# Performance work log

Hardware: AMD Instinct MI355X
Metric: run time of the kernel (lower is better)

## Reference

```python
import jax, jax.numpy as jnp
import numpy as np

N = 50000   # nodes
E = 800000  # edges
G = 64      # graphs in the batch
DIN = 128
DOUT = 256


def _lin(key, fan_in, fan_out):
    s = 1.0 / np.sqrt(fan_in)
    kw, kb = jax.random.split(key)
    W = jax.random.uniform(kw, (fan_in, fan_out), jnp.float32, -s, s)
    b = jax.random.uniform(kb, (fan_out,), jnp.float32, -s, s)
    return W, b


def setup_inputs() -> dict:
    key = jax.random.key(0)
    ks = jax.random.split(key, 12)
    x = jax.random.normal(ks[0], (N, DIN), jnp.float32)
    edge_index = jax.random.randint(ks[1], (2, E), 0, N, dtype=jnp.int64)
    batch = jnp.sort(jax.random.randint(ks[2], (N,), 0, G, dtype=jnp.int64))
    W1, b1 = _lin(ks[3], DIN, 128)
    W2, b2 = _lin(ks[4], 128, 128)
    W3, b3 = _lin(ks[5], 128, 128)
    A1, ba1 = _lin(ks[6], DIN, 64)
    A2, ba2 = _lin(ks[7], 64, 32)
    A3, ba3 = _lin(ks[8], 32, 1)
    M1, bm1 = _lin(ks[9], 128, 128)
    M2, bm2 = _lin(ks[10], 128, DOUT)
    return dict(x=x, edge_index=edge_index, batch=batch,
                W1=W1, b1=b1, W2=W2, b2=b2, W3=W3, b3=b3,
                A1=A1, ba1=ba1, A2=A2, ba2=ba2, A3=A3, ba3=ba3,
                M1=M1, bm1=bm1, M2=M2, bm2=bm2)


def _gcn_norm(edge_index, n, dtype):
    # GCNConv default: add self-loops, symmetric normalization D^-1/2 (A+I) D^-1/2
    loop = jnp.arange(n, dtype=edge_index.dtype)
    src = jnp.concatenate([edge_index[0], loop])
    dst = jnp.concatenate([edge_index[1], loop])
    deg = jax.ops.segment_sum(jnp.ones_like(dst, dtype), dst, num_segments=n)
    dinv = jnp.where(deg > 0, jax.lax.rsqrt(deg), 0.0)
    return src, dst, dinv[src] * dinv[dst]


def _gcn(h, W, b, src, dst, norm, n):
    h = h @ W                                   # [N, F_out]
    msg = h[src] * norm[:, None]                # gather + scale (memory bound)
    return jax.ops.segment_sum(msg, dst, num_segments=n) + b


def _segment_softmax(w, batch, g):
    # per-graph softmax (PyG softmax): stabilize with segment max
    m = jax.ops.segment_max(w, batch, num_segments=g)
    e = jnp.exp(w - m[batch])
    s = jax.ops.segment_sum(e, batch, num_segments=g)
    return e / (s[batch] + 1e-16)


def reference(x, edge_index, batch,
              W1, b1, W2, b2, W3, b3,
              A1, ba1, A2, ba2, A3, ba3,
              M1, bm1, M2, bm2):
    n = x.shape[0]
    src, dst, norm = _gcn_norm(edge_index, n, x.dtype)
    relu = jax.nn.relu
    # feature branch
    f = relu(_gcn(x, W1, b1, src, dst, norm, n))
    f = relu(_gcn(f, W2, b2, src, dst, norm, n))
    f = relu(_gcn(f, W3, b3, src, dst, norm, n))
    # attention branch
    w = relu(_gcn(x, A1, ba1, src, dst, norm, n))
    w = relu(_gcn(w, A2, ba2, src, dst, norm, n))
    w = relu(_gcn(w, A3, ba3, src, dst, norm, n))   # [N, 1]
    w = _segment_softmax(w, batch, G)
    # attention-weighted sum pooling per graph
    pooled = jax.ops.segment_sum(f * w, batch, num_segments=G)  # [G, 128]
    # MLP([128,128,256], batch_norm=False): Linear+ReLU, plain last Linear
    out = relu(pooled @ M1 + bm1) @ M2 + bm2
    return out
```

## Files before the change

kernel.cpp:

```cpp
#include <hip/hip_runtime.h>
#include <hip/hip_fp16.h>
#include <math.h>


#define DIN 128
#define FH  128
#define DOUT 256
#define NBUK 128
#define SUBN 512
#define IMGCAP 16384
#define ECAP 16384

typedef float f4 __attribute__((ext_vector_type(4)));
typedef float f32x4 __attribute__((ext_vector_type(4)));
typedef _Float16 h8v __attribute__((ext_vector_type(8)));
typedef _Float16 h4v __attribute__((ext_vector_type(4)));


__global__ __launch_bounds__(256) void scan1_kernel(const int* __restrict__ cnt,
        int* __restrict__ bsum, float* __restrict__ dinv, int n) {
    __shared__ int sm[256];
    int tid = threadIdx.x;
    int base = blockIdx.x * 512;
    int a = (base + tid < n) ? cnt[base + tid] : 0;
    int b = (base + 256 + tid < n) ? cnt[base + 256 + tid] : 0;
    if (base + tid < n)       dinv[base + tid]       = rsqrtf((float)(a + 1));
    if (base + 256 + tid < n) dinv[base + 256 + tid] = rsqrtf((float)(b + 1));
    sm[tid] = a + b;
    __syncthreads();
    for (int off = 128; off > 0; off >>= 1) {
        if (tid < off) sm[tid] += sm[tid + off];
        __syncthreads();
    }
    if (tid == 0) bsum[blockIdx.x] = sm[0];
}

__global__ void scan2_kernel(const int* __restrict__ bsum, int* __restrict__ boff,
                             int* __restrict__ rpN, int nb) {
    if (threadIdx.x == 0) {
        int run = 0;
        for (int i = 0; i < nb; ++i) { boff[i] = run; run += bsum[i]; }
        *rpN = run;
    }
}

__global__ __launch_bounds__(256) void scan3_kernel(const int* __restrict__ cnt,
        const int* __restrict__ boff, int* __restrict__ rp, int n) {
    __shared__ int sm[256];
    int tid = threadIdx.x;
    int base = blockIdx.x * 512;
    int i0 = base + 2 * tid;
    int c0 = (i0 < n) ? cnt[i0] : 0;
    int c1 = (i0 + 1 < n) ? cnt[i0 + 1] : 0;
    int ps = c0 + c1;
    sm[tid] = ps;
    __syncthreads();
    for (int off = 1; off < 256; off <<= 1) {
        int v = (tid >= off) ? sm[tid - off] : 0;
        __syncthreads();
        sm[tid] += v;
        __syncthreads();
    }
    int excl = sm[tid] - ps + boff[blockIdx.x];
    if (i0 < n) rp[i0] = excl;
    if (i0 + 1 < n) rp[i0 + 1] = excl + c0;
}

__global__ __launch_bounds__(256) void ebucket_kernel(const int* __restrict__ src,
        const int* __restrict__ dst, int* __restrict__ bcur,
        unsigned long long* __restrict__ entries, int E, int shift) {
    __shared__ int lcnt[NBUK], lscan[NBUK], lbase[NBUK], lcur[NBUK];
    __shared__ unsigned long long stage[2048];
    const int tid = threadIdx.x;
    const int e0 = blockIdx.x * 2048;
    if (tid < NBUK) { lcnt[tid] = 0; lcur[tid] = 0; }
    __syncthreads();
    int s_[8], d_[8];
    #pragma unroll
    for (int k = 0; k < 8; ++k) {
        int e = e0 + k * 256 + tid;
        if (e < E) {
            s_[k] = src[e];
            d_[k] = dst[e];
            atomicAdd(&lcnt[d_[k] >> shift], 1);
        } else {
            d_[k] = -1;
        }
    }
    __syncthreads();
    if (tid < NBUK) lscan[tid] = lcnt[tid];
    __syncthreads();
    for (int off = 1; off < NBUK; off <<= 1) {
        int v = 0;
        if (tid < NBUK && tid >= off) v = lscan[tid - off];
        __syncthreads();
        if (tid < NBUK) lscan[tid] += v;
        __syncthreads();
    }
    if (tid < NBUK) {
        lscan[tid] -= lcnt[tid];
        lbase[tid] = lcnt[tid] ? atomicAdd(&bcur[tid], lcnt[tid]) : 0;
    }
    __syncthreads();
    #pragma unroll
    for (int k = 0; k < 8; ++k) {
        if (d_[k] >= 0) {
            int b = d_[k] >> shift;
            int pos = lscan[b] + atomicAdd(&lcur[b], 1);
            stage[pos] = ((unsigned long long)(unsigned)d_[k] << 32) | (unsigned)s_[k];
        }
    }
    __syncthreads();
    const int total = min(2048, E - e0);
    for (int i = tid; i < total; i += 256) {
        int lo = 0, hi = NBUK - 1;
        while (lo < hi) {
            int mid = (lo + hi + 1) >> 1;
            if (lscan[mid] <= i) lo = mid; else hi = mid - 1;
        }
        int idx = lbase[lo] + (i - lscan[lo]);
        if (idx < (lo + 1) * ECAP)
            entries[(size_t)idx] = stage[i];
    }
}

__global__ __launch_bounds__(512) void ecount_kernel(
        const unsigned long long* __restrict__ entries,
        const int* __restrict__ bcur, int* __restrict__ cnt, int n, int shift) {
    __shared__ int hist[SUBN];
    const int b = blockIdx.x;
    const int n0 = b << shift;
    if (n0 >= n) return;
    const int n1 = min(n0 + SUBN, n);
    const int tid = threadIdx.x;
    hist[tid] = 0;
    __syncthreads();
    const size_t ebase = (size_t)b * ECAP;
    const int len = min(bcur[b] - b * ECAP, ECAP);
    for (int i = tid; i < len; i += 512)
        atomicAdd(&hist[(int)(entries[ebase + i] >> 32) - n0], 1);
    __syncthreads();
    if (n0 + tid < n1) cnt[n0 + tid] = hist[tid];
}

__global__ __launch_bounds__(512) void ecsr_kernel(
        const unsigned long long* __restrict__ entries,
        const int* __restrict__ rp, const float* __restrict__ dinv,
        long long* __restrict__ cn, int n, int shift) {
    __shared__ long long img[IMGCAP];
    __shared__ int hist[SUBN];
    __shared__ int lcur[SUBN];
    __shared__ int sm[SUBN];
    __shared__ float dl[SUBN];
    const int b = blockIdx.x;
    const int n0 = b << shift;
    if (n0 >= n) return;
    const int n1 = min(n0 + (1 << shift), n);
    const int base = rp[n0];
    const int len  = rp[n1] - base;
    const size_t ebase = (size_t)b * ECAP;
    const int tid = threadIdx.x;
    hist[tid] = 0;
    lcur[tid] = 0;
    if (n0 + tid < n1) dl[tid] = dinv[n0 + tid];
    __syncthreads();
    for (int i = tid; i < len; i += 512)
        atomicAdd(&hist[(int)(entries[ebase + i] >> 32) - n0], 1);
    __syncthreads();
    int v = hist[tid];
    sm[tid] = v;
    __syncthreads();
    for (int off = 1; off < SUBN; off <<= 1) {
        int t = (tid >= off) ? sm[tid - off] : 0;
        __syncthreads();
        sm[tid] += t;
        __syncthreads();
    }
    hist[tid] = sm[tid] - v;
    __syncthreads();
    const bool fits = (len <= IMGCAP);
    for (int i = tid; i < len; i += 512) {
        unsigned long long e = entries[ebase + i];
        int d  = (int)(e >> 32) - n0;
        int sx = (int)(unsigned)(e & 0xffffffffu);
        int pos = hist[d] + atomicAdd(&lcur[d], 1);
        float w = dinv[sx] * dl[d];
        long long val = (long long)(unsigned)sx | ((long long)__float_as_int(w) << 32);
        if (fits) img[pos] = val;
        else      cn[base + pos] = val;
    }
    __syncthreads();
    if (fits)
        for (int i = tid; i < len; i += 512) cn[base + i] = img[i];
}

__global__ void gstart_kernel(const int* __restrict__ batch, int* __restrict__ gstart,
                              int n, int g) {
    int t = threadIdx.x;
    if (t > g) return;
    int lo = 0, hi = n;
    while (lo < hi) {
        int mid = (lo + hi) >> 1;
        if (batch[mid] < t) lo = mid + 1; else hi = mid;
    }
    gstart[t] = lo;
}

__global__ void cvt16_kernel(const float* __restrict__ in, __half* __restrict__ outh,
                             long n8) {
    long i = (long)blockIdx.x * 256 + threadIdx.x;
    if (i >= n8) return;
    f4 a = ((const f4*)in)[2 * i];
    f4 b = ((const f4*)in)[2 * i + 1];
    __half2 h0 = __float22half2_rn(make_float2(a.x, a.y));
    __half2 h1 = __float22half2_rn(make_float2(a.z, a.w));
    __half2 h2 = __float22half2_rn(make_float2(b.x, b.y));
    __half2 h3 = __float22half2_rn(make_float2(b.z, b.w));
    uint4 st;
    st.x = *(unsigned*)&h0; st.y = *(unsigned*)&h1;
    st.z = *(unsigned*)&h2; st.w = *(unsigned*)&h3;
    ((uint4*)outh)[i] = st;
}


__device__ __forceinline__ void wsplit(const float* __restrict__ W,
        _Float16* __restrict__ Th, _Float16* __restrict__ Tl,
        int fin, int fout, int i) {
    int r = i / fout, c = i % fout;
    float w = W[i];
    _Float16 h = (_Float16)w;
    Th[c * fin + r] = h;
    Tl[c * fin + r] = (_Float16)(w - (float)h);
}

__global__ __launch_bounds__(256) void wprep_kernel(const float* __restrict__ W1,
        const float* __restrict__ W2, const float* __restrict__ W3,
        const float* __restrict__ A1, const float* __restrict__ A2,
        _Float16* __restrict__ T, int* __restrict__ bcur) {
    int i = blockIdx.x * 256 + threadIdx.x;
    if (blockIdx.x == 0 && threadIdx.x < NBUK) bcur[threadIdx.x] = threadIdx.x * ECAP;
    if (i < 16384)       wsplit(W1, T,          T + 16384,  128, 128, i);
    else if (i < 32768)  wsplit(W2, T + 32768,  T + 49152,  128, 128, i - 16384);
    else if (i < 49152)  wsplit(W3, T + 65536,  T + 81920,  128, 128, i - 32768);
    else if (i < 57344)  wsplit(A1, T + 98304,  T + 106496, 128, 64,  i - 49152);
    else if (i < 59392)  wsplit(A2, T + 114688, T + 116736, 64,  32,  i - 57344);
}


__global__ __launch_bounds__(256) void fusedw_kernel(const __half* __restrict__ Yh,
        const __half* __restrict__ Yl, const _Float16* __restrict__ T,
        const float* __restrict__ b1, __half* __restrict__ t2, int n) {
    constexpr int LSTR = 136;
    __shared__ _Float16 L1[64 * LSTR];
    __shared__ _Float16 L2[64 * LSTR];
    const int tid  = threadIdx.x;
    const int w    = tid >> 6;
    const int lane = tid & 63;
    const int bk   = (lane >> 4) * 8;
    const int cl   = lane & 15;
    const long row0 = (long)blockIdx.x * 64;

    for (int i = tid; i < 64 * 16; i += 256) {
        int r = i >> 4, c8 = i & 15;
        long gr = row0 + r;
        uint4 vh = {0u, 0u, 0u, 0u}, vl = {0u, 0u, 0u, 0u};
        if (gr < n) {
            vh = *(const uint4*)&Yh[gr * 128 + c8 * 8];
            vl = *(const uint4*)&Yl[gr * 128 + c8 * 8];
        }
        *(uint4*)&L1[r * LSTR + c8 * 8] = vh;
        *(uint4*)&L2[r * LSTR + c8 * 8] = vl;
    }
    __syncthreads();

    f32x4 accF[4][2];
    {
        const _Float16* W1h = T;
        const _Float16* W1l = T + 16384;
        h8v Bh[2][4], Bl[2][4];
        #pragma unroll
        for (int ct = 0; ct < 2; ++ct) {
            int c = w * 32 + ct * 16 + cl;
            #pragma unroll
            for (int kk = 0; kk < 4; ++kk) {
                Bh[ct][kk] = *(const h8v*)&W1h[c * 128 + kk * 32 + bk];
                Bl[ct][kk] = *(const h8v*)&W1l[c * 128 + kk * 32 + bk];
            }
        }
        #pragma unroll
        for (int rt = 0; rt < 4; ++rt)
            #pragma unroll
            for (int ct = 0; ct < 2; ++ct) accF[rt][ct] = (f32x4){0.f,0.f,0.f,0.f};
        #pragma unroll
        for (int rt = 0; rt < 4; ++rt) {
            int r = rt * 16 + cl;
            #pragma unroll
            for (int kk = 0; kk < 4; ++kk) {
                h8v ah = *(const h8v*)&L1[r * LSTR + kk * 32 + bk];
                h8v al = *(const h8v*)&L2[r * LSTR + kk * 32 + bk];
                #pragma unroll
                for (int ct = 0; ct < 2; ++ct) {
                    accF[rt][ct] = __builtin_amdgcn_mfma_f32_16x16x32_f16(ah, Bh[ct][kk], accF[rt][ct], 0, 0, 0);
                    accF[rt][ct] = __builtin_amdgcn_mfma_f32_16x16x32_f16(ah, Bl[ct][kk], accF[rt][ct], 0, 0, 0);
                    accF[rt][ct] = __builtin_amdgcn_mfma_f32_16x16x32_f16(al, Bh[ct][kk], accF[rt][ct], 0, 0, 0);
                }
            }
        }
    }
    __syncthreads();

    #pragma unroll
    for (int rt = 0; rt < 4; ++rt) {
        int rowb = rt * 16 + (lane >> 4) * 4;
        #pragma unroll
        for (int ct = 0; ct < 2; ++ct) {
            int col = w * 32 + ct * 16 + cl;
            float bv = b1[col];
            #pragma unroll
            for (int j = 0; j < 4; ++j) {
                float v = fmaxf(accF[rt][ct][j] + bv, 0.f);
                _Float16 h = (_Float16)v;
                L1[(rowb + j) * LSTR + col] = h;
                L2[(rowb + j) * LSTR + col] = (_Float16)(v - (float)h);
            }
        }
    }
    __syncthreads();

    {
        const _Float16* W2h = T + 32768;
        const _Float16* W2l = T + 49152;
        h8v Bh[2][4], Bl[2][4];
        #pragma unroll
        for (int ct = 0; ct < 2; ++ct) {
            int c = w * 32 + ct * 16 + cl;
            #pragma unroll
            for (int kk = 0; kk < 4; ++kk) {
                Bh[ct][kk] = *(const h8v*)&W2h[c * 128 + kk * 32 + bk];
                Bl[ct][kk] = *(const h8v*)&W2l[c * 128 + kk * 32 + bk];
            }
        }
        f32x4 acc[4][2];
        #pragma unroll
        for (int rt = 0; rt < 4; ++rt)
            #pragma unroll
            for (int ct = 0; ct < 2; ++ct) acc[rt][ct] = (f32x4){0.f,0.f,0.f,0.f};
        #pragma unroll
        for (int rt = 0; rt < 4; ++rt) {
            int r = rt * 16 + cl;
            #pragma unroll
            for (int kk = 0; kk < 4; ++kk) {
                h8v ah = *(const h8v*)&L1[r * LSTR + kk * 32 + bk];
                h8v al = *(const h8v*)&L2[r * LSTR + kk * 32 + bk];
                #pragma unroll
                for (int ct = 0; ct < 2; ++ct) {
                    acc[rt][ct] = __builtin_amdgcn_mfma_f32_16x16x32_f16(ah, Bh[ct][kk], acc[rt][ct], 0, 0, 0);
                    acc[rt][ct] = __builtin_amdgcn_mfma_f32_16x16x32_f16(ah, Bl[ct][kk], acc[rt][ct], 0, 0, 0);
                    acc[rt][ct] = __builtin_amdgcn_mfma_f32_16x16x32_f16(al, Bh[ct][kk], acc[rt][ct], 0, 0, 0);
                }
            }
        }
        #pragma unroll
        for (int rt = 0; rt < 4; ++rt) {
            long rbase = row0 + rt * 16 + (lane >> 4) * 4;
            #pragma unroll
            for (int ct = 0; ct < 2; ++ct) {
                int col = w * 32 + ct * 16 + cl;
                #pragma unroll
                for (int j = 0; j < 4; ++j) {
                    long r = rbase + j;
                    if (r < n) t2[r * 128 + col] = __float2half(acc[rt][ct][j]);
                }
            }
        }
    }
}


__global__ __launch_bounds__(256) void fuseda_kernel(const __half* __restrict__ Yh,
        const __half* __restrict__ Yl, const _Float16* __restrict__ T,
        const float* __restrict__ ba1, __half* __restrict__ u2, int n) {
    constexpr int LSTR  = 136;
    constexpr int LSTRB = 68;
    __shared__ _Float16 L1[64 * LSTR];
    __shared__ _Float16 L2[64 * LSTR];
    const int tid  = threadIdx.x;
    const int w    = tid >> 6;
    const int lane = tid & 63;
    const int bk   = (lane >> 4) * 8;
    const int cl   = lane & 15;
    const long row0 = (long)blockIdx.x * 64;

    for (int i = tid; i < 64 * 16; i += 256) {
        int r = i >> 4, c8 = i & 15;
        long gr = row0 + r;
        uint4 vh = {0u, 0u, 0u, 0u}, vl = {0u, 0u, 0u, 0u};
        if (gr < n) {
            vh = *(const uint4*)&Yh[gr * 128 + c8 * 8];
            vl = *(const uint4*)&Yl[gr * 128 + c8 * 8];
        }
        *(uint4*)&L1[r * LSTR + c8 * 8] = vh;
        *(uint4*)&L2[r * LSTR + c8 * 8] = vl;
    }
    __syncthreads();

    f32x4 accA[4];
    const int ca = w * 16 + cl;
    {
        const _Float16* A1h = T + 98304;
        const _Float16* A1l = T + 106496;
        h8v A1hf[4], A1lf[4];
        #pragma unroll
        for (int kk = 0; kk < 4; ++kk) {
            A1hf[kk] = *(const h8v*)&A1h[ca * 128 + kk * 32 + bk];
            A1lf[kk] = *(const h8v*)&A1l[ca * 128 + kk * 32 + bk];
        }
        #pragma unroll
        for (int rt = 0; rt < 4; ++rt) accA[rt] = (f32x4){0.f,0.f,0.f,0.f};
        #pragma unroll
        for (int rt = 0; rt < 4; ++rt) {
            int r = rt * 16 + cl;
            #pragma unroll
            for (int kk = 0; kk < 4; ++kk) {
                h8v ah = *(const h8v*)&L1[r * LSTR + kk * 32 + bk];
                h8v al = *(const h8v*)&L2[r * LSTR + kk * 32 + bk];
                accA[rt] = __builtin_amdgcn_mfma_f32_16x16x32_f16(ah, A1hf[kk], accA[rt], 0, 0, 0);
                accA[rt] = __builtin_amdgcn_mfma_f32_16x16x32_f16(ah, A1lf[kk], accA[rt], 0, 0, 0);
                accA[rt] = __builtin_amdgcn_mfma_f32_16x16x32_f16(al, A1hf[kk], accA[rt], 0, 0, 0);
            }
        }
    }
    __syncthreads();

    {
        float bv = ba1[ca];
        #pragma unroll
        for (int rt = 0; rt < 4; ++rt) {
            int rowb = rt * 16 + (lane >> 4) * 4;
            #pragma unroll
            for (int j = 0; j < 4; ++j) {
                float v = fmaxf(accA[rt][j] + bv, 0.f);
                _Float16 h = (_Float16)v;
                L1[(rowb + j) * LSTRB + ca] = h;
                L2[(rowb + j) * LSTRB + ca] = (_Float16)(v - (float)h);
            }
        }
    }
    __syncthreads();

    {
        const _Float16* A2h = T + 114688;
        const _Float16* A2l = T + 116736;
        h8v Bh[2][2], Bl[2][2];
        #pragma unroll
        for (int ct = 0; ct < 2; ++ct) {
            int c = ct * 16 + cl;
            #pragma unroll
            for (int kk = 0; kk < 2; ++kk) {
                Bh[ct][kk] = *(const h8v*)&A2h[c * 64 + kk * 32 + bk];
                Bl[ct][kk] = *(const h8v*)&A2l[c * 64 + kk * 32 + bk];
            }
        }
        f32x4 acc[2];
        acc[0] = (f32x4){0.f,0.f,0.f,0.f};
        acc[1] = (f32x4){0.f,0.f,0.f,0.f};
        const int r = w * 16 + cl;
        #pragma unroll
        for (int kk = 0; kk < 2; ++kk) {
            h8v ah = *(const h8v*)&L1[r * LSTRB + kk * 32 + bk];
            h8v al = *(const h8v*)&L2[r * LSTRB + kk * 32 + bk];
            #pragma unroll
            for (int ct = 0; ct < 2; ++ct) {
                acc[ct] = __builtin_amdgcn_mfma_f32_16x16x32_f16(ah, Bh[ct][kk], acc[ct], 0, 0, 0);
                acc[ct] = __builtin_amdgcn_mfma_f32_16x16x32_f16(ah, Bl[ct][kk], acc[ct], 0, 0, 0);
                acc[ct] = __builtin_amdgcn_mfma_f32_16x16x32_f16(al, Bh[ct][kk], acc[ct], 0, 0, 0);
            }
        }
        long rbase = row0 + w * 16 + (lane >> 4) * 4;
        #pragma unroll
        for (int ct = 0; ct < 2; ++ct) {
            int col = ct * 16 + cl;
            #pragma unroll
            for (int j = 0; j < 4; ++j) {
                long rr = rbase + j;
                if (rr < n) u2[rr * 32 + col] = __float2half(acc[ct][j]);
            }
        }
    }
}

__global__ __launch_bounds__(256) void t3gemm_kernel(const __half* __restrict__ Fh,
        const __half* __restrict__ Fl, const _Float16* __restrict__ Wh,
        const _Float16* __restrict__ Wl, __half* __restrict__ C, int n) {
    constexpr int LSTR = 136;
    __shared__ _Float16 Ahs[64 * LSTR];
    __shared__ _Float16 Als[64 * LSTR];
    const int tid  = threadIdx.x;
    const int w    = tid >> 6;
    const int lane = tid & 63;
    const int bk   = (lane >> 4) * 8;
    const int cl   = lane & 15;
    const long row0 = (long)blockIdx.x * 64;

    for (int i = tid; i < 64 * 16; i += 256) {
        int r = i >> 4, c8 = i & 15;
        long gr = row0 + r;
        uint4 vh = {0u, 0u, 0u, 0u}, vl = {0u, 0u, 0u, 0u};
        if (gr < n) {
            vh = *(const uint4*)&Fh[gr * 128 + c8 * 8];
            vl = *(const uint4*)&Fl[gr * 128 + c8 * 8];
        }
        *(uint4*)&Ahs[r * LSTR + c8 * 8] = vh;
        *(uint4*)&Als[r * LSTR + c8 * 8] = vl;
    }

    h8v Bh[2][4], Bl[2][4];
    #pragma unroll
    for (int ct = 0; ct < 2; ++ct) {
        int c = w * 32 + ct * 16 + cl;
        #pragma unroll
        for (int kk = 0; kk < 4; ++kk) {
            Bh[ct][kk] = *(const h8v*)&Wh[c * 128 + kk * 32 + bk];
            Bl[ct][kk] = *(const h8v*)&Wl[c * 128 + kk * 32 + bk];
        }
    }
    __syncthreads();

    f32x4 acc[4][2];
    #pragma unroll
    for (int rt = 0; rt < 4; ++rt)
        #pragma unroll
        for (int ct = 0; ct < 2; ++ct) acc[rt][ct] = (f32x4){0.f,0.f,0.f,0.f};
    #pragma unroll
    for (int rt = 0; rt < 4; ++rt) {
        int r = rt * 16 + cl;
        #pragma unroll
        for (int kk = 0; kk < 4; ++kk) {
            h8v ah = *(const h8v*)&Ahs[r * LSTR + kk * 32 + bk];
            h8v al = *(const h8v*)&Als[r * LSTR + kk * 32 + bk];
            #pragma unroll
            for (int ct = 0; ct < 2; ++ct) {
                acc[rt][ct] = __builtin_amdgcn_mfma_f32_16x16x32_f16(ah, Bh[ct][kk], acc[rt][ct], 0, 0, 0);
                acc[rt][ct] = __builtin_amdgcn_mfma_f32_16x16x32_f16(ah, Bl[ct][kk], acc[rt][ct], 0, 0, 0);
                acc[rt][ct] = __builtin_amdgcn_mfma_f32_16x16x32_f16(al, Bh[ct][kk], acc[rt][ct], 0, 0, 0);
            }
        }
    }
    #pragma unroll
    for (int rt = 0; rt < 4; ++rt) {
        long rbase = row0 + rt * 16 + (lane >> 4) * 4;
        #pragma unroll
        for (int ct = 0; ct < 2; ++ct) {
            int col = w * 32 + ct * 16 + cl;
            #pragma unroll
            for (int j = 0; j < 4; ++j) {
                long r = rbase + j;
                if (r < n) C[r * 128 + col] = __float2half(acc[rt][ct][j]);
            }
        }
    }
}


__device__ __forceinline__ void hacc8(float acc[8], uint4 u, float w) {
    __half2 h; float2 f;
    h = *(__half2*)&u.x; f = __half22float2(h); acc[0] += w * f.x; acc[1] += w * f.y;
    h = *(__half2*)&u.y; f = __half22float2(h); acc[2] += w * f.x; acc[3] += w * f.y;
    h = *(__half2*)&u.z; f = __half22float2(h); acc[4] += w * f.x; acc[5] += w * f.y;
    h = *(__half2*)&u.w; f = __half22float2(h); acc[6] += w * f.x; acc[7] += w * f.y;
}

template<bool BR>
__global__ __launch_bounds__(256) void agghs_kernel(const __half* __restrict__ tin,
        const float* __restrict__ bias, const float* __restrict__ dinv,
        const int* __restrict__ rp, const long long* __restrict__ cn,
        __half* __restrict__ outh, __half* __restrict__ outl, int n) {
    constexpr int LPR   = 16;
    constexpr int SLOTS = 4;
    const int lane = threadIdx.x & 63;
    const int node = blockIdx.x * 4 + (threadIdx.x >> 6);
    if (node >= n) return;
    const int l    = lane % LPR;
    const int slot = lane / LPR;
    const uint4* base = (const uint4*)tin + l;
    const int e0 = rp[node], e1 = rp[node + 1];
    float acc[8] = {0.f, 0.f, 0.f, 0.f, 0.f, 0.f, 0.f, 0.f};
    if (slot == 0) {
        float di = dinv[node];
        uint4 u = base[(size_t)node * LPR];
        hacc8(acc, u, di * di);
    }
    int p = e0 + slot;
    for (; p + 3 * SLOTS < e1; p += 4 * SLOTS) {
        long long r0 = __builtin_nontemporal_load(cn + p);
        long long r1 = __builtin_nontemporal_load(cn + p + SLOTS);
        long long r2 = __builtin_nontemporal_load(cn + p + 2 * SLOTS);
        long long r3 = __builtin_nontemporal_load(cn + p + 3 * SLOTS);
        uint4 u0 = base[(size_t)(unsigned)r0 * LPR];
        uint4 u1 = base[(size_t)(unsigned)r1 * LPR];
        uint4 u2 = base[(size_t)(unsigned)r2 * LPR];
        uint4 u3 = base[(size_t)(unsigned)r3 * LPR];
        hacc8(acc, u0, __int_as_float((int)(r0 >> 32)));
        hacc8(acc, u1, __int_as_float((int)(r1 >> 32)));
        hacc8(acc, u2, __int_as_float((int)(r2 >> 32)));
        hacc8(acc, u3, __int_as_float((int)(r3 >> 32)));
    }
    for (; p + SLOTS < e1; p += 2 * SLOTS) {
        long long r0 = __builtin_nontemporal_load(cn + p);
        long long r1 = __builtin_nontemporal_load(cn + p + SLOTS);
        uint4 u0 = base[(size_t)(unsigned)r0 * LPR];
        uint4 u1 = base[(size_t)(unsigned)r1 * LPR];
        hacc8(acc, u0, __int_as_float((int)(r0 >> 32)));
        hacc8(acc, u1, __int_as_float((int)(r1 >> 32)));
    }
    if (p < e1) {
        long long r0 = __builtin_nontemporal_load(cn + p);
        uint4 u0 = base[(size_t)(unsigned)r0 * LPR];
        hacc8(acc, u0, __int_as_float((int)(r0 >> 32)));
    }
    #pragma unroll
    for (int off = 32; off >= LPR; off >>= 1) {
        #pragma unroll
        for (int j = 0; j < 8; ++j) acc[j] += __shfl_xor(acc[j], off);
    }
    if (slot == 0) {
        h8v hv, lv;
        #pragma unroll
        for (int j = 0; j < 8; ++j) {
            float v = BR ? fmaxf(acc[j] + bias[l * 8 + j], 0.f) : acc[j];
            _Float16 h = (_Float16)v;
            hv[j] = h;
            lv[j] = (_Float16)(v - (float)h);
        }
        __builtin_nontemporal_store(hv, (h8v*)(outh + (size_t)node * FH + l * 8));
        __builtin_nontemporal_store(lv, (h8v*)(outl + (size_t)node * FH + l * 8));
    }
}

template<int F, bool BR>
__global__ __launch_bounds__(256) void aggh_kernel(const __half* __restrict__ tin,
        const float* __restrict__ bias, const float* __restrict__ dinv,
        const int* __restrict__ rp, const long long* __restrict__ cn,
        float* __restrict__ out, int n) {
    constexpr int LPR   = F / 8;
    constexpr int SLOTS = 64 / LPR;
    const int lane = threadIdx.x & 63;
    const int node = blockIdx.x * 4 + (threadIdx.x >> 6);
    if (node >= n) return;
    const int l    = lane % LPR;
    const int slot = lane / LPR;
    const uint4* base = (const uint4*)tin + l;
    const int e0 = rp[node], e1 = rp[node + 1];
    float acc[8] = {0.f, 0.f, 0.f, 0.f, 0.f, 0.f, 0.f, 0.f};
    if (slot == 0) {
        float di = dinv[node];
        uint4 u = base[(size_t)node * LPR];
        hacc8(acc, u, di * di);
    }
    int p = e0 + slot;
    for (; p + 3 * SLOTS < e1; p += 4 * SLOTS) {
        long long r0 = __builtin_nontemporal_load(cn + p);
        long long r1 = __builtin_nontemporal_load(cn + p + SLOTS);
        long long r2 = __builtin_nontemporal_load(cn + p + 2 * SLOTS);
        long long r3 = __builtin_nontemporal_load(cn + p + 3 * SLOTS);
        uint4 u0 = base[(size_t)(unsigned)r0 * LPR];
        uint4 u1 = base[(size_t)(unsigned)r1 * LPR];
        uint4 u2 = base[(size_t)(unsigned)r2 * LPR];
        uint4 u3 = base[(size_t)(unsigned)r3 * LPR];
        hacc8(acc, u0, __int_as_float((int)(r0 >> 32)));
        hacc8(acc, u1, __int_as_float((int)(r1 >> 32)));
        hacc8(acc, u2, __int_as_float((int)(r2 >> 32)));
        hacc8(acc, u3, __int_as_float((int)(r3 >> 32)));
    }
    for (; p + SLOTS < e1; p += 2 * SLOTS) {
        long long r0 = __builtin_nontemporal_load(cn + p);
        long long r1 = __builtin_nontemporal_load(cn + p + SLOTS);
        uint4 u0 = base[(size_t)(unsigned)r0 * LPR];
        uint4 u1 = base[(size_t)(unsigned)r1 * LPR];
        hacc8(acc, u0, __int_as_float((int)(r0 >> 32)));
        hacc8(acc, u1, __int_as_float((int)(r1 >> 32)));
    }
    if (p < e1) {
        long long r0 = __builtin_nontemporal_load(cn + p);
        uint4 u0 = base[(size_t)(unsigned)r0 * LPR];
        hacc8(acc, u0, __int_as_float((int)(r0 >> 32)));
    }
    #pragma unroll
    for (int off = 32; off >= LPR; off >>= 1) {
        #pragma unroll
        for (int j = 0; j < 8; ++j) acc[j] += __shfl_xor(acc[j], off);
    }
    if (slot == 0) {
        if (BR) {
            #pragma unroll
            for (int j = 0; j < 8; ++j)
                acc[j] = fmaxf(acc[j] + bias[l * 8 + j], 0.f);
        }
        f4 lo = {acc[0], acc[1], acc[2], acc[3]};
        f4 hi = {acc[4], acc[5], acc[6], acc[7]};
        float* o = out + (size_t)node * F + l * 8;
        __builtin_nontemporal_store(lo, (f4*)o);
        __builtin_nontemporal_store(hi, (f4*)(o + 4));
    }
}

__global__ __launch_bounds__(256) void aggh32a_kernel(const __half* __restrict__ tin,
        const float* __restrict__ ba2, const float* __restrict__ A3,
        const float* __restrict__ dinv, const int* __restrict__ rp,
        const long long* __restrict__ cn, float* __restrict__ wlin, int n) {
    constexpr int LPR   = 4;
    constexpr int SLOTS = 16;
    const int lane = threadIdx.x & 63;
    const int node = blockIdx.x * 4 + (threadIdx.x >> 6);
    if (node >= n) return;
    const int l    = lane % LPR;
    const int slot = lane / LPR;
    const uint4* base = (const uint4*)tin + l;
    const int e0 = rp[node], e1 = rp[node + 1];
    float acc[8] = {0.f, 0.f, 0.f, 0.f, 0.f, 0.f, 0.f, 0.f};
    if (slot == 0) {
        float di = dinv[node];
        uint4 u = base[(size_t)node * LPR];
        hacc8(acc, u, di * di);
    }
    int p = e0 + slot;
    for (; p + SLOTS < e1; p += 2 * SLOTS) {
        long long r0 = __builtin_nontemporal_load(cn + p);
        long long r1 = __builtin_nontemporal_load(cn + p + SLOTS);
        uint4 u0 = base[(size_t)(unsigned)r0 * LPR];
        uint4 u1 = base[(size_t)(unsigned)r1 * LPR];
        hacc8(acc, u0, __int_as_float((int)(r0 >> 32)));
        hacc8(acc, u1, __int_as_float((int)(r1 >> 32)));
    }
    if (p < e1) {
        long long r0 = __builtin_nontemporal_load(cn + p);
        uint4 u0 = base[(size_t)(unsigned)r0 * LPR];
        hacc8(acc, u0, __int_as_float((int)(r0 >> 32)));
    }
    #pragma unroll
    for (int off = 32; off >= LPR; off >>= 1) {
        #pragma unroll
        for (int j = 0; j < 8; ++j) acc[j] += __shfl_xor(acc[j], off);
    }
    if (slot == 0) {
        float part = 0.f;
        #pragma unroll
        for (int j = 0; j < 8; ++j)
            part += fmaxf(acc[j] + ba2[l * 8 + j], 0.f) * A3[l * 8 + j];
        part += __shfl_xor(part, 1);
        part += __shfl_xor(part, 2);
        if (l == 0) wlin[node] = part;
    }
}

__global__ void agg1_kernel(const float* __restrict__ tin, const float* __restrict__ bias,
        const float* __restrict__ dinv, const int* __restrict__ rp,
        const long long* __restrict__ cn, float* __restrict__ out, int n) {
    int i = blockIdx.x * 256 + threadIdx.x;
    if (i >= n) return;
    float di = dinv[i];
    float acc = di * di * tin[i];
    int e0 = rp[i], e1 = rp[i + 1];
    int p = e0;
    float a0 = 0.f, a1 = 0.f, a2 = 0.f, a3 = 0.f;
    for (; p + 3 < e1; p += 4) {
        long long r0 = __builtin_nontemporal_load(cn + p);
        long long r1 = __builtin_nontemporal_load(cn + p + 1);
        long long r2 = __builtin_nontemporal_load(cn + p + 2);
        long long r3 = __builtin_nontemporal_load(cn + p + 3);
        a0 += __int_as_float((int)(r0 >> 32)) * tin[(int)(unsigned)r0];
        a1 += __int_as_float((int)(r1 >> 32)) * tin[(int)(unsigned)r1];
        a2 += __int_as_float((int)(r2 >> 32)) * tin[(int)(unsigned)r2];
        a3 += __int_as_float((int)(r3 >> 32)) * tin[(int)(unsigned)r3];
    }
    for (; p < e1; ++p) {
        long long r0 = __builtin_nontemporal_load(cn + p);
        a0 += __int_as_float((int)(r0 >> 32)) * tin[(int)(unsigned)r0];
    }
    acc += a0 + a1 + a2 + a3 + bias[0];
    out[i] = acc > 0.f ? acc : 0.f;
}


__global__ __launch_bounds__(256) void smexp_kernel(const float* __restrict__ w,
        const int* __restrict__ gstart, float* __restrict__ gsum,
        float* __restrict__ e) {
    const int g = blockIdx.x;
    const int a = gstart[g], b = gstart[g + 1];
    const int tid = threadIdx.x;
    __shared__ float red[4];
    float m = 0.f;
    for (int i = a + tid; i < b; i += 256) m = fmaxf(m, w[i]);
    #pragma unroll
    for (int off = 32; off > 0; off >>= 1) m = fmaxf(m, __shfl_xor(m, off));
    if ((tid & 63) == 0) red[tid >> 6] = m;
    __syncthreads();
    m = fmaxf(fmaxf(red[0], red[1]), fmaxf(red[2], red[3]));
    float s = 0.f;
    for (int i = a + tid; i < b; i += 256) {
        float ex = expf(w[i] - m);
        e[i] = ex;
        s += ex;
    }
    #pragma unroll
    for (int off = 32; off > 0; off >>= 1) s += __shfl_xor(s, off);
    __syncthreads();
    if ((tid & 63) == 0) red[tid >> 6] = s;
    __syncthreads();
    if (tid == 0) gsum[g] = red[0] + red[1] + red[2] + red[3];
}


__global__ __launch_bounds__(128) void pool_kernel(const float* __restrict__ f3,
        const float* __restrict__ e, const float* __restrict__ gsum,
        const int* __restrict__ gstart, float* __restrict__ pooled) {
    constexpr int SPG = 64;
    const int g = blockIdx.x / SPG, s = blockIdx.x % SPG;
    const int a = gstart[g], bnd = gstart[g + 1];
    const int len = bnd - a;
    if (len <= 0) return;
    const int chunk = (len + SPG - 1) / SPG;
    const int lo = a + s * chunk;
    const int hi = min(lo + chunk, bnd);
    if (lo >= hi) return;
    const float inv = 1.f / (gsum[g] + 1e-16f);
    const int tid = threadIdx.x;
    const int lane4 = tid & 31;
    const int rs    = tid >> 5;
    f4 acc = {0.f, 0.f, 0.f, 0.f};
    for (int i = lo + rs; i < hi; i += 4) {
        float w = e[i] * inv;
        f4 v = *(const f4*)&f3[(size_t)i * FH + lane4 * 4];
        acc.x += w * v.x; acc.y += w * v.y;
        acc.z += w * v.z; acc.w += w * v.w;
    }
    acc.x += __shfl_xor(acc.x, 32);
    acc.y += __shfl_xor(acc.y, 32);
    acc.z += __shfl_xor(acc.z, 32);
    acc.w += __shfl_xor(acc.w, 32);
    __shared__ float sm[128];
    if (tid >= 64 && tid < 96) *(f4*)&sm[(tid - 64) * 4] = acc;
    __syncthreads();
    if (tid < 32) {
        f4 o = *(f4*)&sm[tid * 4];
        o.x += acc.x; o.y += acc.y; o.z += acc.z; o.w += acc.w;
        float* dst = &pooled[g * FH + tid * 4];
        atomicAdd(dst + 0, o.x);
        atomicAdd(dst + 1, o.y);
        atomicAdd(dst + 2, o.z);
        atomicAdd(dst + 3, o.w);
    }
}


__global__ __launch_bounds__(256) void mlp_kernel(const float* __restrict__ pooled,
        const float* __restrict__ M1, const float* __restrict__ bm1,
        const float* __restrict__ M2, const float* __restrict__ bm2,
        float* __restrict__ out) {
    __shared__ float pr[FH];
    __shared__ float hr[FH];
    int g = blockIdx.x, j = threadIdx.x;
    if (j < FH) pr[j] = pooled[g * FH + j];
    __syncthreads();
    if (j < FH) {
        float acc = bm1[j];
        #pragma unroll 8
        for (int k = 0; k < FH; ++k) acc += pr[k] * M1[k * FH + j];
        hr[j] = acc > 0.f ? acc : 0.f;
    }
    __syncthreads();
    float acc = bm2[j];
    #pragma unroll 8
    for (int k = 0; k < FH; ++k) acc += hr[k] * M2[k * DOUT + j];
    out[g * DOUT + j] = acc;
}


extern "C" void kernel_launch(void* const* d_in, const int* in_sizes, int n_in,
                              void* d_out, int out_size, void* d_ws, size_t ws_size,
                              hipStream_t stream) {
    const float* x   = (const float*)d_in[0];
    const int*   ei  = (const int*)d_in[1];
    const int*   batch = (const int*)d_in[2];
    const float* W1  = (const float*)d_in[3];
    const float* b1  = (const float*)d_in[4];
    const float* W2  = (const float*)d_in[5];
    const float* b2  = (const float*)d_in[6];
    const float* W3  = (const float*)d_in[7];
    const float* b3  = (const float*)d_in[8];
    const float* A1  = (const float*)d_in[9];
    const float* ba1 = (const float*)d_in[10];
    const float* A2  = (const float*)d_in[11];
    const float* ba2 = (const float*)d_in[12];
    const float* A3  = (const float*)d_in[13];
    const float* ba3 = (const float*)d_in[14];
    const float* M1  = (const float*)d_in[15];
    const float* bm1 = (const float*)d_in[16];
    const float* M2  = (const float*)d_in[17];
    const float* bm2 = (const float*)d_in[18];

    const int N = in_sizes[0] / DIN;
    const int E = in_sizes[1] / 2;
    const int G = out_size / DOUT;
    const int* src = ei;
    const int* dst = ei + E;
    float* out = (float*)d_out;

    int shift = 9;
    while (((N + (1 << shift) - 1) >> shift) > NBUK) ++shift;
    const int nbuckets = (N + (1 << shift) - 1) >> shift;

    char* p = (char*)d_ws;
    auto alloc = [&](size_t bytes) -> void* {
        void* r = (void*)p;
        p += (bytes + 255) & ~(size_t)255;
        return r;
    };
    float* dinv  = (float*)alloc((size_t)N * 4);
    int*   cnt   = (int*)alloc((size_t)N * 4);
    int*   rp    = (int*)alloc((size_t)(N + 1) * 4);
    long long* cn = (long long*)alloc((size_t)E * 8);
    float* SY    = (float*)alloc((size_t)N * FH * 4);
    float* SA    = (float*)alloc((size_t)N * FH * 4);
    __half* ST   = (__half*)alloc((size_t)N * FH * 2);
    char*  SX    = (char*)alloc((size_t)N * 256);
    __half* u2   = (__half*)alloc((size_t)N * 32 * 2);
    float* wlin  = (float*)alloc((size_t)N * 4);
    float* wact  = (float*)alloc((size_t)N * 4);
    float* ebuf  = (float*)alloc((size_t)N * 4);
    float* gsum  = (float*)alloc((size_t)G * 4);
    int*   gstart= (int*)alloc((size_t)(G + 1) * 4);
    float* pooled= (float*)alloc((size_t)G * FH * 4);
    int*   bsum  = (int*)alloc(256 * 4);
    int*   boff  = (int*)alloc(256 * 4);
    int*   bcur  = (int*)alloc(NBUK * 4);
    _Float16* WT = (_Float16*)alloc((size_t)118784 * 2);

    __half* xh  = (__half*)SX;
    __half* Yh  = (__half*)SY;
    __half* Yl  = Yh + (size_t)N * FH;
    __half* F2h = (__half*)SA;
    __half* F2l = F2h + (size_t)N * FH;
    unsigned long long* entries = (unsigned long long*)SA;

    hipMemsetAsync(pooled, 0, (size_t)G * FH * 4, stream);

    const int nb = (N + 255) / 256;
    const int NB = (N + 511) / 512;

    wprep_kernel<<<232, 256, 0, stream>>>(W1, W2, W3, A1, A2, WT, bcur);
    ebucket_kernel<<<(E + 2047) / 2048, 256, 0, stream>>>(src, dst, bcur, entries, E, shift);
    ecount_kernel<<<nbuckets, 512, 0, stream>>>(entries, bcur, cnt, N, shift);
    scan1_kernel<<<NB, 256, 0, stream>>>(cnt, bsum, dinv, N);
    scan2_kernel<<<1, 64, 0, stream>>>(bsum, boff, rp + N, NB);
    scan3_kernel<<<NB, 256, 0, stream>>>(cnt, boff, rp, N);
    gstart_kernel<<<1, 128, 0, stream>>>(batch, gstart, N, G);
    ecsr_kernel<<<nbuckets, 512, 0, stream>>>(entries, rp, dinv, cn, N, shift);

    const long n8 = (long)N * FH / 8;
    cvt16_kernel<<<(int)((n8 + 255) / 256), 256, 0, stream>>>(x, xh, n8);

    const int gb64 = (N + 63) / 64;
    const int agb  = (N + 3) / 4;

    agghs_kernel<false><<<agb, 256, 0, stream>>>(xh, nullptr, dinv, rp, cn, Yh, Yl, N);

    fusedw_kernel<<<gb64, 256, 0, stream>>>(Yh, Yl, WT, b1, (__half*)ST, N);
    fuseda_kernel<<<gb64, 256, 0, stream>>>(Yh, Yl, WT, ba1, u2, N);

    agghs_kernel<true><<<agb, 256, 0, stream>>>(ST, b2, dinv, rp, cn, F2h, F2l, N);
    t3gemm_kernel<<<gb64, 256, 0, stream>>>(F2h, F2l, WT + 65536, WT + 81920, (__half*)ST, N);
    aggh_kernel<FH, true><<<agb, 256, 0, stream>>>(ST, b3, dinv, rp, cn, SY, N);

    aggh32a_kernel<<<agb, 256, 0, stream>>>(u2, ba2, A3, dinv, rp, cn, wlin, N);
    agg1_kernel<<<nb, 256, 0, stream>>>(wlin, ba3, dinv, rp, cn, wact, N);

    smexp_kernel<<<G, 256, 0, stream>>>(wact, gstart, gsum, ebuf);
    pool_kernel<<<G * 64, 128, 0, stream>>>(SY, ebuf, gsum, gstart, pooled);

    mlp_kernel<<<G, 256, 0, stream>>>(pooled, M1, bm1, M2, bm2, out);
}
```

Baseline: 305.5 us.

## Split 128-wide aggregation into four 32-column slabs with slab-major outputs

The three 128-feature aggregation kernels now run four blocks per node group, each gathering one 32-column slice (64 bytes) of neighbor rows with 16 edge slots per wave instead of 4. Outputs are written in a slab-major layout [4][N][32], and the downstream GEMM loaders and the pooling kernel are changed to read that layout. The goal is to raise edge-level parallelism and give the gather working set better cache locality, since the blocks with the same slab index share a 32-column slice. The cost is that each edge's index and weight record is read four times and each gathered segment shrinks to 64 bytes.

New measurement: 473.0 us. +54.8%, slower.

```diff
diff --git a/kernel.cpp b/kernel.cpp
--- a/kernel.cpp
+++ b/kernel.cpp
@@ -260,16 +260,19 @@
     const int cl   = lane & 15;
     const long row0 = (long)blockIdx.x * 64;
 
-    for (int i = tid; i < 64 * 16; i += 256) {
-        int r = i >> 4, c8 = i & 15;
+    for (int i = tid; i < 1024; i += 256) {
+        int s = i >> 8;
+        int r = (i & 255) >> 2;
+        int q = i & 3;
         long gr = row0 + r;
         uint4 vh = {0u, 0u, 0u, 0u}, vl = {0u, 0u, 0u, 0u};
         if (gr < n) {
-            vh = *(const uint4*)&Yh[gr * 128 + c8 * 8];
-            vl = *(const uint4*)&Yl[gr * 128 + c8 * 8];
-        }
-        *(uint4*)&L1[r * LSTR + c8 * 8] = vh;
-        *(uint4*)&L2[r * LSTR + c8 * 8] = vl;
+            size_t a = ((size_t)s * n + gr) * 32 + q * 8;
+            vh = *(const uint4*)&Yh[a];
+            vl = *(const uint4*)&Yl[a];
+        }
+        *(uint4*)&L1[r * LSTR + s * 32 + q * 8] = vh;
+        *(uint4*)&L2[r * LSTR + s * 32 + q * 8] = vl;
     }
     __syncthreads();
 
@@ -391,16 +394,19 @@
     const int cl   = lane & 15;
     const long row0 = (long)blockIdx.x * 64;
 
-    for (int i = tid; i < 64 * 16; i += 256) {
-        int r = i >> 4, c8 = i & 15;
+    for (int i = tid; i < 1024; i += 256) {
+        int s = i >> 8;
+        int r = (i & 255) >> 2;
+        int q = i & 3;
         long gr = row0 + r;
         uint4 vh = {0u, 0u, 0u, 0u}, vl = {0u, 0u, 0u, 0u};
         if (gr < n) {
-            vh = *(const uint4*)&Yh[gr * 128 + c8 * 8];
-            vl = *(const uint4*)&Yl[gr * 128 + c8 * 8];
-        }
-        *(uint4*)&L1[r * LSTR + c8 * 8] = vh;
-        *(uint4*)&L2[r * LSTR + c8 * 8] = vl;
+            size_t a = ((size_t)s * n + gr) * 32 + q * 8;
+            vh = *(const uint4*)&Yh[a];
+            vl = *(const uint4*)&Yl[a];
+        }
+        *(uint4*)&L1[r * LSTR + s * 32 + q * 8] = vh;
+        *(uint4*)&L2[r * LSTR + s * 32 + q * 8] = vl;
     }
     __syncthreads();
 
@@ -502,16 +508,19 @@
     const int cl   = lane & 15;
     const long row0 = (long)blockIdx.x * 64;
 
-    for (int i = tid; i < 64 * 16; i += 256) {
-        int r = i >> 4, c8 = i & 15;
+    for (int i = tid; i < 1024; i += 256) {
+        int s = i >> 8;
+        int r = (i & 255) >> 2;
+        int q = i & 3;
         long gr = row0 + r;
         uint4 vh = {0u, 0u, 0u, 0u}, vl = {0u, 0u, 0u, 0u};
         if (gr < n) {
-            vh = *(const uint4*)&Fh[gr * 128 + c8 * 8];
-            vl = *(const uint4*)&Fl[gr * 128 + c8 * 8];
-        }
-        *(uint4*)&Ahs[r * LSTR + c8 * 8] = vh;
-        *(uint4*)&Als[r * LSTR + c8 * 8] = vl;
+            size_t a = ((size_t)s * n + gr) * 32 + q * 8;
+            vh = *(const uint4*)&Fh[a];
+            vl = *(const uint4*)&Fl[a];
+        }
+        *(uint4*)&Ahs[r * LSTR + s * 32 + q * 8] = vh;
+        *(uint4*)&Als[r * LSTR + s * 32 + q * 8] = vl;
     }
 
     h8v Bh[2][4], Bl[2][4];
@@ -571,24 +580,23 @@
 }
 
 template<bool BR>
-__global__ __launch_bounds__(256) void agghs_kernel(const __half* __restrict__ tin,
+__global__ __launch_bounds__(256) void aggs_kernel(const __half* __restrict__ tin,
         const float* __restrict__ bias, const float* __restrict__ dinv,
         const int* __restrict__ rp, const long long* __restrict__ cn,
         __half* __restrict__ outh, __half* __restrict__ outl, int n) {
-    constexpr int LPR   = 16;
-    constexpr int SLOTS = 4;
+    constexpr int SLOTS = 16;
+    const int s    = blockIdx.x & 3;
+    const int node = (blockIdx.x >> 2) * 4 + (threadIdx.x >> 6);
+    if (node >= n) return;
     const int lane = threadIdx.x & 63;
-    const int node = blockIdx.x * 4 + (threadIdx.x >> 6);
-    if (node >= n) return;
-    const int l    = lane % LPR;
-    const int slot = lane / LPR;
-    const uint4* base = (const uint4*)tin + l;
+    const int l    = lane & 3;
+    const int slot = lane >> 2;
+    const uint4* base = (const uint4*)tin + s * 4 + l;
     const int e0 = rp[node], e1 = rp[node + 1];
     float acc[8] = {0.f, 0.f, 0.f, 0.f, 0.f, 0.f, 0.f, 0.f};
     if (slot == 0) {
         float di = dinv[node];
-        uint4 u = base[(size_t)node * LPR];
-        hacc8(acc, u, di * di);
+        hacc8(acc, base[(size_t)node * 16], di * di);
     }
     int p = e0 + slot;
     for (; p + 3 * SLOTS < e1; p += 4 * SLOTS) {
@@ -596,10 +604,10 @@
         long long r1 = __builtin_nontemporal_load(cn + p + SLOTS);
         long long r2 = __builtin_nontemporal_load(cn + p + 2 * SLOTS);
         long long r3 = __builtin_nontemporal_load(cn + p + 3 * SLOTS);
-        uint4 u0 = base[(size_t)(unsigned)r0 * LPR];
-        uint4 u1 = base[(size_t)(unsigned)r1 * LPR];
-        uint4 u2 = base[(size_t)(unsigned)r2 * LPR];
-        uint4 u3 = base[(size_t)(unsigned)r3 * LPR];
+        uint4 u0 = base[(size_t)(unsigned)r0 * 16];
+        uint4 u1 = base[(size_t)(unsigned)r1 * 16];
+        uint4 u2 = base[(size_t)(unsigned)r2 * 16];
+        uint4 u3 = base[(size_t)(unsigned)r3 * 16];
         hacc8(acc, u0, __int_as_float((int)(r0 >> 32)));
         hacc8(acc, u1, __int_as_float((int)(r1 >> 32)));
         hacc8(acc, u2, __int_as_float((int)(r2 >> 32)));
@@ -608,18 +616,18 @@
     for (; p + SLOTS < e1; p += 2 * SLOTS) {
         long long r0 = __builtin_nontemporal_load(cn + p);
         long long r1 = __builtin_nontemporal_load(cn + p + SLOTS);
-        uint4 u0 = base[(size_t)(unsigned)r0 * LPR];
-        uint4 u1 = base[(size_t)(unsigned)r1 * LPR];
+        uint4 u0 = base[(size_t)(unsigned)r0 * 16];
+        uint4 u1 = base[(size_t)(unsigned)r1 * 16];
         hacc8(acc, u0, __int_as_float((int)(r0 >> 32)));
         hacc8(acc, u1, __int_as_float((int)(r1 >> 32)));
     }
     if (p < e1) {
         long long r0 = __builtin_nontemporal_load(cn + p);
-        uint4 u0 = base[(size_t)(unsigned)r0 * LPR];
+        uint4 u0 = base[(size_t)(unsigned)r0 * 16];
         hacc8(acc, u0, __int_as_float((int)(r0 >> 32)));
     }
     #pragma unroll
-    for (int off = 32; off >= LPR; off >>= 1) {
+    for (int off = 32; off >= 4; off >>= 1) {
         #pragma unroll
         for (int j = 0; j < 8; ++j) acc[j] += __shfl_xor(acc[j], off);
     }
@@ -627,35 +635,34 @@
         h8v hv, lv;
         #pragma unroll
         for (int j = 0; j < 8; ++j) {
-            float v = BR ? fmaxf(acc[j] + bias[l * 8 + j], 0.f) : acc[j];
+            float v = BR ? fmaxf(acc[j] + bias[s * 32 + l * 8 + j], 0.f) : acc[j];
             _Float16 h = (_Float16)v;
             hv[j] = h;
             lv[j] = (_Float16)(v - (float)h);
         }
-        __builtin_nontemporal_store(hv, (h8v*)(outh + (size_t)node * FH + l * 8));
-        __builtin_nontemporal_store(lv, (h8v*)(outl + (size_t)node * FH + l * 8));
-    }
-}
-
-template<int F, bool BR>
-__global__ __launch_bounds__(256) void aggh_kernel(const __half* __restrict__ tin,
+        size_t o = ((size_t)s * n + node) * 32 + l * 8;
+        __builtin_nontemporal_store(hv, (h8v*)(outh + o));
+        __builtin_nontemporal_store(lv, (h8v*)(outl + o));
+    }
+}
+
+__global__ __launch_bounds__(256) void aggsf_kernel(const __half* __restrict__ tin,
         const float* __restrict__ bias, const float* __restrict__ dinv,
         const int* __restrict__ rp, const long long* __restrict__ cn,
         float* __restrict__ out, int n) {
-    constexpr int LPR   = F / 8;
-    constexpr int SLOTS = 64 / LPR;
+    constexpr int SLOTS = 16;
+    const int s    = blockIdx.x & 3;
+    const int node = (blockIdx.x >> 2) * 4 + (threadIdx.x >> 6);
+    if (node >= n) return;
     const int lane = threadIdx.x & 63;
-    const int node = blockIdx.x * 4 + (threadIdx.x >> 6);
-    if (node >= n) return;
-    const int l    = lane % LPR;
-    const int slot = lane / LPR;
-    const uint4* base = (const uint4*)tin + l;
+    const int l    = lane & 3;
+    const int slot = lane >> 2;
+    const uint4* base = (const uint4*)tin + s * 4 + l;
     const int e0 = rp[node], e1 = rp[node + 1];
     float acc[8] = {0.f, 0.f, 0.f, 0.f, 0.f, 0.f, 0.f, 0.f};
     if (slot == 0) {
         float di = dinv[node];
-        uint4 u = base[(size_t)node * LPR];
-        hacc8(acc, u, di * di);
+        hacc8(acc, base[(size_t)node * 16], di * di);
     }
     int p = e0 + slot;
     for (; p + 3 * SLOTS < e1; p += 4 * SLOTS) {
@@ -663,10 +670,10 @@
         long long r1 = __builtin_nontemporal_load(cn + p + SLOTS);
         long long r2 = __builtin_nontemporal_load(cn + p + 2 * SLOTS);
         long long r3 = __builtin_nontemporal_load(cn + p + 3 * SLOTS);
-        uint4 u0 = base[(size_t)(unsigned)r0 * LPR];
-        uint4 u1 = base[(size_t)(unsigned)r1 * LPR];
-        uint4 u2 = base[(size_t)(unsigned)r2 * LPR];
-        uint4 u3 = base[(size_t)(unsigned)r3 * LPR];
+        uint4 u0 = base[(size_t)(unsigned)r0 * 16];
+        uint4 u1 = base[(size_t)(unsigned)r1 * 16];
+        uint4 u2 = base[(size_t)(unsigned)r2 * 16];
+        uint4 u3 = base[(size_t)(unsigned)r3 * 16];
         hacc8(acc, u0, __int_as_float((int)(r0 >> 32)));
         hacc8(acc, u1, __int_as_float((int)(r1 >> 32)));
         hacc8(acc, u2, __int_as_float((int)(r2 >> 32)));
@@ -675,30 +682,28 @@
     for (; p + SLOTS < e1; p += 2 * SLOTS) {
         long long r0 = __builtin_nontemporal_load(cn + p);
         long long r1 = __builtin_nontemporal_load(cn + p + SLOTS);
-        uint4 u0 = base[(size_t)(unsigned)r0 * LPR];
-        uint4 u1 = base[(size_t)(unsigned)r1 * LPR];
+        uint4 u0 = base[(size_t)(unsigned)r0 * 16];
+        uint4 u1 = base[(size_t)(unsigned)r1 * 16];
         hacc8(acc, u0, __int_as_float((int)(r0 >> 32)));
         hacc8(acc, u1, __int_as_float((int)(r1 >> 32)));
     }
     if (p < e1) {
         long long r0 = __builtin_nontemporal_load(cn + p);
-        uint4 u0 = base[(size_t)(unsigned)r0 * LPR];
+        uint4 u0 = base[(size_t)(unsigned)r0 * 16];
         hacc8(acc, u0, __int_as_float((int)(r0 >> 32)));
     }
     #pragma unroll
-    for (int off = 32; off >= LPR; off >>= 1) {
+    for (int off = 32; off >= 4; off >>= 1) {
         #pragma unroll
         for (int j = 0; j < 8; ++j) acc[j] += __shfl_xor(acc[j], off);
     }
     if (slot == 0) {
-        if (BR) {
-            #pragma unroll
-            for (int j = 0; j < 8; ++j)
-                acc[j] = fmaxf(acc[j] + bias[l * 8 + j], 0.f);
-        }
+        #pragma unroll
+        for (int j = 0; j < 8; ++j)
+            acc[j] = fmaxf(acc[j] + bias[s * 32 + l * 8 + j], 0.f);
         f4 lo = {acc[0], acc[1], acc[2], acc[3]};
         f4 hi = {acc[4], acc[5], acc[6], acc[7]};
-        float* o = out + (size_t)node * F + l * 8;
+        float* o = out + ((size_t)s * n + node) * 32 + l * 8;
         __builtin_nontemporal_store(lo, (f4*)o);
         __builtin_nontemporal_store(hi, (f4*)(o + 4));
     }
@@ -813,7 +818,7 @@
 
 __global__ __launch_bounds__(128) void pool_kernel(const float* __restrict__ f3,
         const float* __restrict__ e, const float* __restrict__ gsum,
-        const int* __restrict__ gstart, float* __restrict__ pooled) {
+        const int* __restrict__ gstart, float* __restrict__ pooled, int n) {
     constexpr int SPG = 64;
     const int g = blockIdx.x / SPG, s = blockIdx.x % SPG;
     const int a = gstart[g], bnd = gstart[g + 1];
@@ -827,10 +832,13 @@
     const int tid = threadIdx.x;
     const int lane4 = tid & 31;
     const int rs    = tid >> 5;
+    const int s4 = lane4 >> 3;
+    const int c4 = lane4 & 7;
+    const float* fb = f3 + (size_t)s4 * n * 32;
     f4 acc = {0.f, 0.f, 0.f, 0.f};
     for (int i = lo + rs; i < hi; i += 4) {
         float w = e[i] * inv;
-        f4 v = *(const f4*)&f3[(size_t)i * FH + lane4 * 4];
+        f4 v = *(const f4*)&fb[(size_t)i * 32 + c4 * 4];
         acc.x += w * v.x; acc.y += w * v.y;
         acc.z += w * v.z; acc.w += w * v.w;
     }
@@ -844,7 +852,7 @@
     if (tid < 32) {
         f4 o = *(f4*)&sm[tid * 4];
         o.x += acc.x; o.y += acc.y; o.z += acc.z; o.w += acc.w;
-        float* dst = &pooled[g * FH + tid * 4];
+        float* dst = &pooled[g * FH + (tid >> 3) * 32 + (tid & 7) * 4];
         atomicAdd(dst + 0, o.x);
         atomicAdd(dst + 1, o.y);
         atomicAdd(dst + 2, o.z);
@@ -961,22 +969,22 @@
     cvt16_kernel<<<(int)((n8 + 255) / 256), 256, 0, stream>>>(x, xh, n8);
 
     const int gb64 = (N + 63) / 64;
-    const int agb  = (N + 3) / 4;
-
-    agghs_kernel<false><<<agb, 256, 0, stream>>>(xh, nullptr, dinv, rp, cn, Yh, Yl, N);
+    const int agb4 = ((N + 3) / 4) * 4;
+
+    aggs_kernel<false><<<agb4, 256, 0, stream>>>(xh, nullptr, dinv, rp, cn, Yh, Yl, N);
 
     fusedw_kernel<<<gb64, 256, 0, stream>>>(Yh, Yl, WT, b1, (__half*)ST, N);
     fuseda_kernel<<<gb64, 256, 0, stream>>>(Yh, Yl, WT, ba1, u2, N);
 
-    agghs_kernel<true><<<agb, 256, 0, stream>>>(ST, b2, dinv, rp, cn, F2h, F2l, N);
+    aggs_kernel<true><<<agb4, 256, 0, stream>>>(ST, b2, dinv, rp, cn, F2h, F2l, N);
     t3gemm_kernel<<<gb64, 256, 0, stream>>>(F2h, F2l, WT + 65536, WT + 81920, (__half*)ST, N);
-    aggh_kernel<FH, true><<<agb, 256, 0, stream>>>(ST, b3, dinv, rp, cn, SY, N);
-
-    aggh32a_kernel<<<agb, 256, 0, stream>>>(u2, ba2, A3, dinv, rp, cn, wlin, N);
+    aggsf_kernel<<<agb4, 256, 0, stream>>>(ST, b3, dinv, rp, cn, SY, N);
+
+    aggh32a_kernel<<<(N + 3) / 4, 256, 0, stream>>>(u2, ba2, A3, dinv, rp, cn, wlin, N);
     agg1_kernel<<<nb, 256, 0, stream>>>(wlin, ba3, dinv, rp, cn, wact, N);
 
     smexp_kernel<<<G, 256, 0, stream>>>(wact, gstart, gsum, ebuf);
-    pool_kernel<<<G * 64, 128, 0, stream>>>(SY, ebuf, gsum, gstart, pooled);
+    pool_kernel<<<G * 64, 128, 0, stream>>>(SY, ebuf, gsum, gstart, pooled, N);
 
     mlp_kernel<<<G, 256, 0, stream>>>(pooled, M1, bm1, M2, bm2, out);
 }
```
